# Optimization experiments

Measured on AMD Instinct MI355X. Metric: run time of the kernel, lower is better.

## Reference

```python
import jax, jax.numpy as jnp
import numpy as np

B, CIN, COUT, H, W = 16, 128, 128, 64, 64
K1, K2, DIL = 3, 3, 1
PAD0 = DIL * (K1 - 1) // 2
PAD1 = DIL * (K2 - 1) // 2
L = H * W


def setup_inputs() -> dict:
    key = jax.random.key(0)
    k1, k2, k3, k4, k5 = jax.random.split(key, 5)
    x = jax.random.normal(k1, (B, CIN, H, W), dtype=jnp.float32)
    # binary per-pixel mask over kernel taps, broadcast over batch*channels
    mask = (jax.random.uniform(k2, (1, K1 * K2, L)) < 0.5).astype(jnp.float32)
    fan_in = CIN * K1 * K2
    bound = 1.0 / np.sqrt(fan_in)
    weight = jax.random.uniform(k3, (COUT, CIN, K1, K2), jnp.float32, -bound, bound)
    mask_weight = jax.random.uniform(k4, (COUT, K1, K2), jnp.float32, -bound, bound)
    bias = jax.random.uniform(k5, (COUT,), jnp.float32, -bound, bound)
    return {"x": x, "mask": mask, "weight": weight, "mask_weight": mask_weight, "bias": bias}


def reference(x, mask, weight, mask_weight, bias):
    # im2col: [B, CIN*K1*K2, H, W]; channel ordering (cin, k1, k2) matches torch unfold
    patches = jax.lax.conv_general_dilated_patches(
        x, (K1, K2), (1, 1), [(PAD0, PAD0), (PAD1, PAD1)], rhs_dilation=(DIL, DIL))
    p = patches.reshape(B, CIN, K1 * K2, L)
    p = p * mask[:, None, :, :]          # mask [1, K, L] broadcasts over B and CIN
    p = p.reshape(B, CIN * K1 * K2, L)
    out = jnp.einsum('ok,bkl->bol', weight.reshape(COUT, -1), p)
    out = out + bias[None, :, None]
    out = out + jnp.einsum('ok,mkl->mol', mask_weight.reshape(COUT, -1), mask)
    return out.reshape(B, COUT, H, W)
```

## Files before the change

kernel.cpp:

```cpp
#include <hip/hip_runtime.h>
#include <stdint.h>

#define B_    16
#define CIN_  128
#define COUT_ 128
#define H_    64
#define W_    64
#define L_    4096
#define KK_   1152
#define PW_   66

typedef unsigned short u16;
typedef __bf16 bf16x8 __attribute__((ext_vector_type(8)));
typedef float  floatx4 __attribute__((ext_vector_type(4)));
typedef uint32_t u32x4 __attribute__((ext_vector_type(4)));

typedef const __attribute__((address_space(1))) uint32_t* gptr_t;
typedef __attribute__((address_space(3))) uint32_t*       lptr_t;

__device__ __forceinline__ void async_copy16(const void* g, void* l) {
    __builtin_amdgcn_global_load_lds((gptr_t)g, (lptr_t)l, 16, 0, 0);
}

__device__ __forceinline__ u16 f2bf(float f) {
    uint32_t u = __builtin_bit_cast(uint32_t, f);
    uint32_t r = u + 0x7FFFu + ((u >> 16) & 1u);
    return (u16)(r >> 16);
}

__global__ void lmc_pre_kernel(const float* __restrict__ x, u16* __restrict__ xTp,
                               const float* __restrict__ mask, const float* __restrict__ mw,
                               const float* __restrict__ bias, const float* __restrict__ w,
                               float* __restrict__ mb, u16* __restrict__ wb2) {
    __shared__ u16 tile[64][CIN_ + 8];
    const int tid = threadIdx.x;

    if (blockIdx.y == 16) {
        const int bid = blockIdx.x;
        const int base = bid * 2304;
        #pragma unroll
        for (int i = 0; i < 9; ++i) {
            const int e = base + i * 256 + tid;
            const int k = e >> 14;
            const int rem = e & 16383;
            const int o = rem >> 7, c = rem & 127;
            wb2[e] = f2bf(w[(size_t)o * KK_ + c * 9 + k]);
        }
        #pragma unroll
        for (int oo = 0; oo < 2; ++oo) {
            const int o = bid * 2 + oo;
            float m[9];
            #pragma unroll
            for (int k = 0; k < 9; ++k) m[k] = mw[o * 9 + k];
            const float bs = bias[o];
            for (int l = tid; l < L_; l += 256) {
                float s = bs;
                #pragma unroll
                for (int k = 0; k < 9; ++k) s += m[k] * mask[k * L_ + l];
                mb[o * L_ + l] = s;
            }
        }
        return;
    }

    const int b = blockIdx.y;
    const int y = blockIdx.x;
    {
        const int c  = tid >> 1;
        const int x0 = (tid & 1) * 32;
        const float* src = x + ((size_t)b * CIN_ + c) * L_ + y * 64 + x0;
        #pragma unroll
        for (int j = 0; j < 32; j += 4) {
            float4 v = *reinterpret_cast<const float4*>(src + j);
            tile[x0 + j + 0][c] = f2bf(v.x);
            tile[x0 + j + 1][c] = f2bf(v.y);
            tile[x0 + j + 2][c] = f2bf(v.z);
            tile[x0 + j + 3][c] = f2bf(v.w);
        }
    }
    __syncthreads();

    u16* dstrow = xTp + ((size_t)(b * PW_ + (y + 1)) * PW_) * CIN_;
    {
        const int xx   = tid >> 2;
        const int cseg = (tid & 3) * 32;
        u16* dst = dstrow + (size_t)(xx + 1) * CIN_ + cseg;
        #pragma unroll
        for (int i = 0; i < 32; i += 8) {
            *reinterpret_cast<uint4*>(dst + i) =
                *reinterpret_cast<const uint4*>(&tile[xx][cseg + i]);
        }
    }
    const uint4 z = {0u, 0u, 0u, 0u};
    if (tid < 32) {
        const int pix = (tid >> 4) ? 65 : 0;
        *reinterpret_cast<uint4*>(dstrow + (size_t)pix * CIN_ + (tid & 15) * 8) = z;
    }
    if (y == 0 || y == 63) {
        u16* brow = xTp + ((size_t)(b * PW_ + (y == 0 ? 0 : 65)) * PW_) * CIN_;
        for (int i = tid; i < (PW_ * CIN_) / 8; i += 256)
            reinterpret_cast<uint4*>(brow)[i] = z;
    }
}

__global__ __launch_bounds__(256, 2)
void lmc_gemm_kernel(const u16* __restrict__ xTp, const u16* __restrict__ wb2,
                     const float* __restrict__ mask, const float* __restrict__ mb,
                     float* __restrict__ out) {
    __shared__ u16 Bwin[4 * 64 * 128];

    const int b    = blockIdx.y;
    const int tile = blockIdx.x;
    const int l0   = tile * 128;
    const int tid  = threadIdx.x;
    const int lane = tid & 63;
    const int wv   = tid >> 6;
    const int wm   = (wv >> 1) * 64;
    const int wn   = (wv & 1) * 64;
    const int lrow = lane & 15;
    const int quad = lane >> 4;

    {
        const char* srcrow = (const char*)xTp
            + ((size_t)((b * PW_) + tile * 2 + wv) * PW_ + 1) * 256;
        char* dst = (char*)Bwin + wv * 16384;
        const int cl = lane >> 4;
        #pragma unroll
        for (int seg = 0; seg < 16; ++seg) {
            const int col = seg * 4 + cl;
            const int ch  = (lane & 15) ^ (col & 7);
            async_copy16(srcrow + col * 256 + ch * 16, dst + seg * 1024);
        }
    }

    uint64_t bits = 0;
    #pragma unroll
    for (int j = 0; j < 4; ++j) {
        const int xl  = j * 16 + lrow;
        const int l_g = l0 + wn + xl;
        #pragma unroll
        for (int k = 0; k < 9; ++k) {
            const int dx = k - (k / 3) * 3 - 1;
            const bool xok = (unsigned)(xl + dx) < 64u;
            if (xok && mask[k * L_ + l_g] != 0.0f) bits |= (1ull << (k * 4 + j));
        }
    }

    floatx4 acc[4][4];
    #pragma unroll
    for (int i = 0; i < 4; ++i)
        #pragma unroll
        for (int j = 0; j < 4; ++j)
            acc[i][j] = (floatx4){0.f, 0.f, 0.f, 0.f};

    int rowA[4];
    #pragma unroll
    for (int i = 0; i < 4; ++i) rowA[i] = (wm + i * 16 + lrow) * 256 + quad * 16;
    const int ywave = wn >> 6;
    const char* wb2_c = (const char*)wb2;
    const char* Bw = (const char*)Bwin;

    __syncthreads();

    for (int k = 0; k < 9; ++k) {
        const int dy = k / 3 - 1;
        const int dx = k - (k / 3) * 3 - 1;
        const char* Ak = wb2_c + k * 32768;
        const int rowbase = (ywave + 1 + dy) * 16384;

        int baddr[4], c7[4];
        #pragma unroll
        for (int j = 0; j < 4; ++j) {
            int col = j * 16 + lrow + dx;
            col = min(max(col, 0), 63);
            baddr[j] = rowbase + col * 256;
            c7[j] = col & 7;
        }
        uint32_t kp[4];
        #pragma unroll
        for (int j = 0; j < 4; ++j)
            kp[j] = 0u - (uint32_t)((bits >> (k * 4 + j)) & 1ull);

        #pragma unroll
        for (int ks = 0; ks < 4; ++ks) {
            bf16x8 af[4], bfr[4];
            #pragma unroll
            for (int i = 0; i < 4; ++i)
                af[i] = *reinterpret_cast<const bf16x8*>(Ak + rowA[i] + ks * 64);
            #pragma unroll
            for (int j = 0; j < 4; ++j) {
                const int slot = ((ks * 4 + quad) ^ c7[j]) * 16;
                bf16x8 v = *reinterpret_cast<const bf16x8*>(Bw + baddr[j] + slot);
                u32x4 t = __builtin_bit_cast(u32x4, v);
                t &= kp[j];
                bfr[j] = __builtin_bit_cast(bf16x8, t);
            }
            #pragma unroll
            for (int i = 0; i < 4; ++i)
                #pragma unroll
                for (int j = 0; j < 4; ++j)
                    acc[i][j] = __builtin_amdgcn_mfma_f32_16x16x32_bf16(af[i], bfr[j], acc[i][j], 0, 0, 0);
        }
    }

    #pragma unroll
    for (int i = 0; i < 4; ++i) {
        #pragma unroll
        for (int j = 0; j < 4; ++j) {
            const int l = l0 + wn + j * 16 + lrow;
            #pragma unroll
            for (int r = 0; r < 4; ++r) {
                const int o = wm + i * 16 + quad * 4 + r;
                out[((size_t)b * COUT_ + o) * L_ + l] = acc[i][j][r] + mb[o * L_ + l];
            }
        }
    }
}

extern "C" void kernel_launch(void* const* d_in, const int* in_sizes, int n_in,
                              void* d_out, int out_size, void* d_ws, size_t ws_size,
                              hipStream_t stream) {
    const float* x      = (const float*)d_in[0];
    const float* mask   = (const float*)d_in[1];
    const float* weight = (const float*)d_in[2];
    const float* mw     = (const float*)d_in[3];
    const float* bias   = (const float*)d_in[4];
    float* out = (float*)d_out;

    char* ws = (char*)d_ws;
    u16*   xTp = (u16*)ws;
    u16*   wb2 = (u16*)(ws + 17842176);
    float* mb  = (float*)(ws + 17842176 + 294912);

    lmc_pre_kernel<<<dim3(64, 17), 256, 0, stream>>>(x, xTp, mask, mw, bias, weight, mb, wb2);
    lmc_gemm_kernel<<<dim3(32, 16), 256, 0, stream>>>(xTp, wb2, mask, mb, out);
}
```

Baseline: 145.1 us.

## Stage weight tiles into LDS and shrink GEMM blocks to one image row

The GEMM kernel now has each block cover one output row (64 pixels) with two waves, instead of two rows with four waves. It loads the 3-row input window in two 64-channel halves. Weight tiles for each tap are copied asynchronously into swizzled LDS rather than read straight from global memory per MFMA. This trades direct global/L2 weight reads for LDS reads, but adds many block-wide barriers, and staging is serialized with compute without double buffering. The grid doubles while per-block LDS and wave count shrink, which changes occupancy.

After: 143.0 us. Within noise of the previous version (-1.4%).

```diff
diff --git a/kernel.cpp b/kernel.cpp
--- a/kernel.cpp
+++ b/kernel.cpp
@@ -103,46 +103,58 @@
     }
 }
 
-__global__ __launch_bounds__(256, 2)
+__global__ __launch_bounds__(128, 2)
 void lmc_gemm_kernel(const u16* __restrict__ xTp, const u16* __restrict__ wb2,
                      const float* __restrict__ mask, const float* __restrict__ mb,
                      float* __restrict__ out) {
-    __shared__ u16 Bwin[4 * 64 * 128];
+    __shared__ u16 Bwin[3 * 64 * 64];
+    __shared__ u16 A_lds[128 * 64];
 
     const int b    = blockIdx.y;
-    const int tile = blockIdx.x;
-    const int l0   = tile * 128;
+    const int yrow = blockIdx.x;
+    const int l0   = yrow << 6;
     const int tid  = threadIdx.x;
     const int lane = tid & 63;
     const int wv   = tid >> 6;
-    const int wm   = (wv >> 1) * 64;
-    const int wn   = (wv & 1) * 64;
     const int lrow = lane & 15;
     const int quad = lane >> 4;
-
-    {
-        const char* srcrow = (const char*)xTp
-            + ((size_t)((b * PW_) + tile * 2 + wv) * PW_ + 1) * 256;
-        char* dst = (char*)Bwin + wv * 16384;
-        const int cl = lane >> 4;
-        #pragma unroll
-        for (int seg = 0; seg < 16; ++seg) {
-            const int col = seg * 4 + cl;
-            const int ch  = (lane & 15) ^ (col & 7);
-            async_copy16(srcrow + col * 256 + ch * 16, dst + seg * 1024);
-        }
-    }
+    const int wm   = wv << 6;
+
+    const char* xTp_c = (const char*)xTp;
+    const char* wb2_c = (const char*)wb2;
+    char* Bw = (char*)Bwin;
+    char* Al = (char*)A_lds;
+    const size_t browbase = ((size_t)(b * PW_) + yrow) * PW_ * 256;
+
+    auto stageB = [&](int ch) {
+        #pragma unroll
+        for (int seg = 0; seg < 12; ++seg) {
+            const int p   = wv * 96 + seg * 8 + (lane >> 3);
+            const int row = p >> 6, col = p & 63;
+            const char* g = xTp_c + browbase + ((size_t)row * PW_ + 1 + col) * 256
+                            + ch * 128 + (((lane & 7) ^ (col & 7)) << 4);
+            async_copy16(g, Bw + (wv * 96 + seg * 8) * 128);
+        }
+    };
+    auto stageA = [&](int t, int ch) {
+        #pragma unroll
+        for (int seg = 0; seg < 8; ++seg) {
+            const int o = wv * 64 + seg * 8 + (lane >> 3);
+            const char* g = wb2_c + t * 32768 + o * 256 + ch * 128
+                            + (((lane & 7) ^ (o & 7)) << 4);
+            async_copy16(g, Al + (wv * 64 + seg * 8) * 128);
+        }
+    };
 
     uint64_t bits = 0;
     #pragma unroll
     for (int j = 0; j < 4; ++j) {
-        const int xl  = j * 16 + lrow;
-        const int l_g = l0 + wn + xl;
+        const int xl = j * 16 + lrow;
         #pragma unroll
         for (int k = 0; k < 9; ++k) {
             const int dx = k - (k / 3) * 3 - 1;
             const bool xok = (unsigned)(xl + dx) < 64u;
-            if (xok && mask[k * L_ + l_g] != 0.0f) bits |= (1ull << (k * 4 + j));
+            if (xok && mask[k * L_ + l0 + xl] != 0.0f) bits |= (1ull << (k * 4 + j));
         }
     }
 
@@ -153,44 +165,34 @@
         for (int j = 0; j < 4; ++j)
             acc[i][j] = (floatx4){0.f, 0.f, 0.f, 0.f};
 
-    int rowA[4];
-    #pragma unroll
-    for (int i = 0; i < 4; ++i) rowA[i] = (wm + i * 16 + lrow) * 256 + quad * 16;
-    const int ywave = wn >> 6;
-    const char* wb2_c = (const char*)wb2;
-    const char* Bw = (const char*)Bwin;
-
-    __syncthreads();
-
-    for (int k = 0; k < 9; ++k) {
+    const int o7 = lrow & 7;
+
+    auto comp = [&](int k) {
         const int dy = k / 3 - 1;
         const int dx = k - (k / 3) * 3 - 1;
-        const char* Ak = wb2_c + k * 32768;
-        const int rowbase = (ywave + 1 + dy) * 16384;
-
+        const int rowbase = (1 + dy) * 8192;
         int baddr[4], c7[4];
+        uint32_t kp[4];
         #pragma unroll
         for (int j = 0; j < 4; ++j) {
             int col = j * 16 + lrow + dx;
             col = min(max(col, 0), 63);
-            baddr[j] = rowbase + col * 256;
+            baddr[j] = rowbase + col * 128;
             c7[j] = col & 7;
-        }
-        uint32_t kp[4];
-        #pragma unroll
-        for (int j = 0; j < 4; ++j)
             kp[j] = 0u - (uint32_t)((bits >> (k * 4 + j)) & 1ull);
-
-        #pragma unroll
-        for (int ks = 0; ks < 4; ++ks) {
+        }
+        #pragma unroll
+        for (int ks = 0; ks < 2; ++ks) {
+            const int ch = ks * 4 + quad;
             bf16x8 af[4], bfr[4];
             #pragma unroll
             for (int i = 0; i < 4; ++i)
-                af[i] = *reinterpret_cast<const bf16x8*>(Ak + rowA[i] + ks * 64);
+                af[i] = *reinterpret_cast<const bf16x8*>(
+                    Al + (wm + i * 16 + lrow) * 128 + ((ch ^ o7) << 4));
             #pragma unroll
             for (int j = 0; j < 4; ++j) {
-                const int slot = ((ks * 4 + quad) ^ c7[j]) * 16;
-                bf16x8 v = *reinterpret_cast<const bf16x8*>(Bw + baddr[j] + slot);
+                bf16x8 v = *reinterpret_cast<const bf16x8*>(
+                    Bw + baddr[j] + ((ch ^ c7[j]) << 4));
                 u32x4 t = __builtin_bit_cast(u32x4, v);
                 t &= kp[j];
                 bfr[j] = __builtin_bit_cast(bf16x8, t);
@@ -199,7 +201,29 @@
             for (int i = 0; i < 4; ++i)
                 #pragma unroll
                 for (int j = 0; j < 4; ++j)
-                    acc[i][j] = __builtin_amdgcn_mfma_f32_16x16x32_bf16(af[i], bfr[j], acc[i][j], 0, 0, 0);
+                    acc[i][j] = __builtin_amdgcn_mfma_f32_16x16x32_bf16(
+                        af[i], bfr[j], acc[i][j], 0, 0, 0);
+        }
+    };
+
+    stageB(0);
+    stageA(0, 0);
+    __syncthreads();
+
+    #pragma unroll
+    for (int ch = 0; ch < 2; ++ch) {
+        #pragma unroll
+        for (int k = 0; k < 9; ++k) {
+            comp(k);
+            __syncthreads();
+            if (k < 8) {
+                stageA(k + 1, ch);
+                __syncthreads();
+            } else if (ch == 0) {
+                stageB(1);
+                stageA(0, 1);
+                __syncthreads();
+            }
         }
     }
 
@@ -207,7 +231,7 @@
     for (int i = 0; i < 4; ++i) {
         #pragma unroll
         for (int j = 0; j < 4; ++j) {
-            const int l = l0 + wn + j * 16 + lrow;
+            const int l = l0 + j * 16 + lrow;
             #pragma unroll
             for (int r = 0; r < 4; ++r) {
                 const int o = wm + i * 16 + quad * 4 + r;
@@ -233,5 +257,5 @@
     float* mb  = (float*)(ws + 17842176 + 294912);
 
     lmc_pre_kernel<<<dim3(64, 17), 256, 0, stream>>>(x, xTp, mask, mw, bias, weight, mb, wb2);
-    lmc_gemm_kernel<<<dim3(32, 16), 256, 0, stream>>>(xTp, wb2, mask, mb, out);
-}
+    lmc_gemm_kernel<<<dim3(64, 16), 128, 0, stream>>>(xTp, wb2, mask, mb, out);
+}
```
